# Kernel tuning notes

Hardware: AMD Instinct MI355X
Metric: run time of the kernel (lower is better)

Reference implementation:

```python
import jax, jax.numpy as jnp
import numpy as np
from jax import lax

B, CIN, COUT, LAT, H, W, K = 16, 512, 512, 512, 32, 32, 3


def setup_inputs() -> dict:
    key = jax.random.key(0)
    k1, k2, k3, k4 = jax.random.split(key, 4)
    return {
        "x": jax.random.normal(k1, (B, CIN, H, W), jnp.float32),
        "w": jax.random.normal(k2, (B, LAT), jnp.float32),
        "weight": jax.random.normal(k3, (COUT, CIN, K, K), jnp.float32) * 0.05,
        "bias": jnp.zeros((1, COUT, 1, 1), jnp.float32),
        "affine_w": jax.random.normal(k4, (CIN, LAT), jnp.float32) * 0.02,
        "affine_b": jnp.zeros((CIN,), jnp.float32),
    }


def _blur_kernel():
    # make_kernel([1,3,3,1]) * upsample_factor**2 (factor=2)
    k = jnp.array([1.0, 3.0, 3.0, 1.0], jnp.float32)
    k = k[None, :] * k[:, None]
    k = k / k.sum()
    return k * 4.0  # (4, 4)


def reference(x, w, weight, bias, affine_w, affine_b):
    bs = x.shape[0]
    # style: affine(w) + 1  -> (B, Cin)
    s = w @ affine_w.T + affine_b + 1.0
    # per-sample modulated weights (B, Cout, Cin, K, K)
    wm = s[:, None, :, None, None] * weight[None]
    # demodulation
    d = lax.rsqrt(jnp.sum(wm * wm, axis=(2, 3, 4)) + 1e-8)  # (B, Cout)
    wm = d[:, :, None, None, None] * wm
    # fused grouped conv_transpose2d(stride=2, padding=0) expressed as a
    # direct cross-correlation with lhs_dilation=2, pad K-1, spatially
    # flipped per-sample kernels, feature_group_count = batch.
    rhs = jnp.flip(wm, (-2, -1)).reshape(bs * COUT, CIN, K, K)
    xr = x.reshape(1, bs * CIN, H, W)
    y = lax.conv_general_dilated(
        xr, rhs, window_strides=(1, 1),
        padding=((K - 1, K - 1), (K - 1, K - 1)),
        lhs_dilation=(2, 2),
        dimension_numbers=("NCHW", "OIHW", "NCHW"),
        feature_group_count=bs)
    Ho, Wo = y.shape[2], y.shape[3]  # 65, 65
    y = y.reshape(bs, COUT, Ho, Wo)
    # upfirdn2d blur: up=1, down=1, pad=(1,1); torch correlates with the
    # flipped kernel, i.e. a true convolution -> depthwise correlate flipped k.
    bk = jnp.flip(_blur_kernel(), (0, 1))
    dw = jnp.broadcast_to(bk[None, None], (COUT, 1, 4, 4))
    y = lax.conv_general_dilated(
        y, dw, window_strides=(1, 1), padding=((1, 1), (1, 1)),
        dimension_numbers=("NCHW", "OIHW", "NCHW"),
        feature_group_count=COUT)  # -> (B, Cout, 64, 64)
    return y + bias
```

## Files before the change

kernel.cpp:

```cpp
#include <hip/hip_runtime.h>

#define CIN  512
#define COUT 512
#define LAT  512
#define NB   16

typedef __attribute__((ext_vector_type(8))) short bf16x8;
typedef __attribute__((ext_vector_type(4))) float f32x4;

__device__ __forceinline__ unsigned short f2bf(float f) {
    unsigned int u = __builtin_bit_cast(unsigned int, f);
    u += 0x7FFFu + ((u >> 16) & 1u);
    return (unsigned short)(u >> 16);
}

__global__ void k_style(const float* __restrict__ w, const float* __restrict__ aw,
                        const float* __restrict__ ab, float* __restrict__ s) {
    int b = blockIdx.x, ci = threadIdx.x;
    __shared__ float wl[LAT];
    wl[ci] = w[b * LAT + ci];
    __syncthreads();
    const float4* awr = (const float4*)(aw + (size_t)ci * LAT);
    float acc = 0.f;
#pragma unroll 4
    for (int l = 0; l < LAT / 4; ++l) {
        float4 a4 = awr[l];
        const float* wp = &wl[l * 4];
        acc += a4.x * wp[0] + a4.y * wp[1] + a4.z * wp[2] + a4.w * wp[3];
    }
    s[b * CIN + ci] = acc + ab[ci] + 1.0f;
}

__global__ void k_wsq(const float* __restrict__ weight, float* __restrict__ wsq) {
    int co = blockIdx.x, ci = threadIdx.x;
    const float* p = weight + ((size_t)co * CIN + ci) * 9;
    float a = 0.f;
#pragma unroll
    for (int k = 0; k < 9; ++k) a += p[k] * p[k];
    wsq[co * CIN + ci] = a;
}

__global__ void k_demod(const float* __restrict__ s, const float* __restrict__ wsq,
                        float* __restrict__ d) {
    int b = blockIdx.x, co = threadIdx.x;
    __shared__ float s2[CIN];
    float sv = s[b * CIN + co];
    s2[co] = sv * sv;
    __syncthreads();
    const float4* wr = (const float4*)(wsq + (size_t)co * CIN);
    float acc = 0.f;
#pragma unroll 4
    for (int i = 0; i < CIN / 4; ++i) {
        float4 v = wr[i];
        const float* sp = &s2[i * 4];
        acc += v.x * sp[0] + v.y * sp[1] + v.z * sp[2] + v.w * sp[3];
    }
    d[b * COUT + co] = rsqrtf(acc + 1e-8f);
}

__global__ void k_prepw(const float* __restrict__ weight, unsigned short* __restrict__ A9) {
    int co = blockIdx.x, t = threadIdx.x;
    __shared__ float wl[CIN * 9];
    const float* wp = weight + (size_t)co * CIN * 9;
    for (int i = t; i < CIN * 9; i += 256) wl[i] = wp[i];
    __syncthreads();
    unsigned short* ap = A9 + (size_t)co * 9 * CIN;
    for (int i = t; i < CIN * 9; i += 256) {
        int kk = i >> 9, ci = i & 511;
        ap[i] = f2bf(wl[ci * 9 + kk]);
    }
}

__global__ void k_prepx(const float* __restrict__ x, const float* __restrict__ s,
                        unsigned short* __restrict__ XT) {
    int blk = blockIdx.x;
    int b = blk >> 7, pt = (blk >> 3) & 15, ct = blk & 7;
    int p0 = pt * 64, ci0 = ct * 64;
    __shared__ float xt[64][65];
    __shared__ float ss[64];
    int t = threadIdx.x;
    if (t < 64) ss[t] = s[b * CIN + ci0 + t];
    const float* xb = x + ((size_t)(b * CIN + ci0)) * 1024 + p0;
#pragma unroll
    for (int rr = 0; rr < 4; ++rr) {
        int i = rr * 16 + (t >> 4), j = (t & 15) * 4;
        float4 v = *(const float4*)(xb + (size_t)i * 1024 + j);
        xt[i][j] = v.x; xt[i][j + 1] = v.y; xt[i][j + 2] = v.z; xt[i][j + 3] = v.w;
    }
    __syncthreads();
    unsigned short* xo = XT + ((size_t)(b * 1024 + p0)) * CIN + ci0;
#pragma unroll
    for (int rr = 0; rr < 4; ++rr) {
        int jj = rr * 16 + (t >> 4);
        int c4 = (t & 15) * 4;
        ushort4 o;
        o.x = f2bf(xt[c4][jj] * ss[c4]);
        o.y = f2bf(xt[c4 + 1][jj] * ss[c4 + 1]);
        o.z = f2bf(xt[c4 + 2][jj] * ss[c4 + 2]);
        o.w = f2bf(xt[c4 + 3][jj] * ss[c4 + 3]);
        *(ushort4*)(xo + (size_t)jj * CIN + c4) = o;
    }
}

__device__ __forceinline__ void gload16(const void* g, void* l) {
    __builtin_amdgcn_global_load_lds(
        (const __attribute__((address_space(1))) void*)g,
        (__attribute__((address_space(3))) void*)l, 16, 0, 0);
}

__device__ __forceinline__ unsigned int swz_goff(unsigned int o) {
    unsigned int row = o >> 6, kb = o & 63u;
    unsigned int kbx = kb ^ (((row >> 1) & 3u) << 4);
    return row * 1024u + kbx;
}

__launch_bounds__(256, 3)
__global__ void k_gemm(const unsigned short* __restrict__ A9,
                       const unsigned short* __restrict__ XT,
                       _Float16* __restrict__ C, int Ns) {
    __shared__ unsigned short smem[8192];
    const int t = threadIdx.x;
    const int bm = blockIdx.x, bn = blockIdx.y;

    const unsigned int o0 = (unsigned)t * 16u;
    const unsigned int o1 = o0 + 4096u;
    char* lA0 = (char*)smem + ((t >> 6) * 1024);
    char* lA1 = lA0 + 4096;
    char* lB0 = lA0 + 8192;
    char* lB1 = lA1 + 8192;
    const char* gA = (const char*)A9 + (size_t)bm * 128 * 1024;
    const char* gB = (const char*)XT + (size_t)bn * 128 * 1024;
    const char* pA0 = gA + swz_goff(o0);
    const char* pA1 = gA + swz_goff(o1);
    const char* pB0 = gB + swz_goff(o0);
    const char* pB1 = gB + swz_goff(o1);

    const int lane = t & 63, w = t >> 6, wr = w >> 1, wc = w & 1;
    const int lrow = lane & 15;
    const unsigned int kbx = (unsigned)(((lane >> 4) << 4) ^ (((lrow >> 1) & 3) << 4));
    unsigned int offA[4], offB[4];
#pragma unroll
    for (int f = 0; f < 4; ++f) {
        offA[f] = (unsigned)((wr * 64 + f * 16 + lrow) * 64) + kbx;
        offB[f] = 8192u + (unsigned)((wc * 64 + f * 16 + lrow) * 64) + kbx;
    }

    f32x4 acc[4][4];
#pragma unroll
    for (int i = 0; i < 4; ++i)
#pragma unroll
        for (int j = 0; j < 4; ++j) acc[i][j] = (f32x4){0.f, 0.f, 0.f, 0.f};

    for (int it = 0; it < 16; ++it) {
        __syncthreads();
        gload16(pA0, lA0); gload16(pA1, lA1);
        gload16(pB0, lB0); gload16(pB1, lB1);
        pA0 += 64; pA1 += 64; pB0 += 64; pB1 += 64;
        __syncthreads();
        bf16x8 a[4], b[4];
#pragma unroll
        for (int f = 0; f < 4; ++f) a[f] = *(const bf16x8*)((const char*)smem + offA[f]);
#pragma unroll
        for (int f = 0; f < 4; ++f) b[f] = *(const bf16x8*)((const char*)smem + offB[f]);
#pragma unroll
        for (int mf = 0; mf < 4; ++mf)
#pragma unroll
            for (int nf = 0; nf < 4; ++nf)
                acc[mf][nf] = __builtin_amdgcn_mfma_f32_16x16x32_bf16(
                    a[mf], b[nf], acc[mf][nf], 0, 0, 0);
    }

    const int mg0 = bm * 128 + wr * 64 + (lane >> 4) * 4;
    const int ng0 = bn * 128 + wc * 64 + (lane & 15);
#pragma unroll
    for (int mf = 0; mf < 4; ++mf)
#pragma unroll
        for (int j = 0; j < 4; ++j) {
            size_t row = (size_t)(mg0 + mf * 16 + j) * (size_t)Ns;
#pragma unroll
            for (int nf = 0; nf < 4; ++nf)
                C[row + ng0 + nf * 16] = (_Float16)acc[mf][nf][j];
        }
}

__global__ void k_scat(const _Float16* __restrict__ C, const float* __restrict__ dmod,
                       const float* __restrict__ bias, float* __restrict__ out,
                       int b0, int Ns) {
    const int blk = blockIdx.x;
    const int bl = blk >> 9, co = blk & 511, b = b0 + bl;
    const int t = threadIdx.x;
    __shared__ _Float16 ct[9][1024];
    __shared__ float ys[67 * 68];

    const _Float16* Cb = C + (size_t)(co * 9) * (size_t)Ns + bl * 1024;
#pragma unroll
    for (int k = 0; k < 9; ++k)
        ((ushort4*)ct[k])[t] = ((const ushort4*)(Cb + (size_t)k * Ns))[t];
    for (int i = t; i < 67 * 68; i += 256) ys[i] = 0.f;
    __syncthreads();

    for (int id = t; id < 65 * 65; id += 256) {
        int oy = id / 65, ox = id - oy * 65;
        int kys[2], iys[2], nk = 0;
        if (oy & 1) { kys[0] = 1; iys[0] = oy >> 1; nk = 1; }
        else {
            int h = oy >> 1;
            if (h < 32) { kys[0] = 0; iys[0] = h; nk = 1; }
            if (h >= 1) { kys[nk] = 2; iys[nk] = h - 1; nk++; }
        }
        int kxs[2], ixs[2], nx = 0;
        if (ox & 1) { kxs[0] = 1; ixs[0] = ox >> 1; nx = 1; }
        else {
            int h = ox >> 1;
            if (h < 32) { kxs[0] = 0; ixs[0] = h; nx = 1; }
            if (h >= 1) { kxs[nx] = 2; ixs[nx] = h - 1; nx++; }
        }
        float v = 0.f;
        for (int ia = 0; ia < nk; ++ia)
            for (int ic = 0; ic < nx; ++ic)
                v += (float)ct[kys[ia] * 3 + kxs[ic]][iys[ia] * 32 + ixs[ic]];
        ys[(oy + 1) * 68 + ox + 1] = v;
    }
    __syncthreads();

    const float dv = dmod[b * COUT + co];
    const float bv = bias[co];
    const int px = t & 63, py0 = t >> 6;
    float* orow = out + ((size_t)b * COUT + co) * 4096;
    const float kv[4] = {0.25f, 0.75f, 0.75f, 0.25f};
#pragma unroll 4
    for (int j = 0; j < 16; ++j) {
        int py = py0 + 4 * j;
        float sum = 0.f;
#pragma unroll
        for (int u = 0; u < 4; ++u) {
            const float* yr = &ys[(py + u) * 68 + px];
            float rs = yr[0] * kv[0] + yr[1] * kv[1] + yr[2] * kv[2] + yr[3] * kv[3];
            sum = fmaf(rs, kv[u], sum);
        }
        orow[py * 64 + px] = dv * sum + bv;
    }
}

extern "C" void kernel_launch(void* const* d_in, const int* in_sizes, int n_in,
                              void* d_out, int out_size, void* d_ws, size_t ws_size,
                              hipStream_t stream) {
    const float* x      = (const float*)d_in[0];
    const float* w      = (const float*)d_in[1];
    const float* weight = (const float*)d_in[2];
    const float* bias   = (const float*)d_in[3];
    const float* aw     = (const float*)d_in[4];
    const float* ab     = (const float*)d_in[5];
    float* out = (float*)d_out;

    char* wsb = (char*)d_ws;
    float* s            = (float*)wsb;
    float* dmod         = (float*)(wsb + 32768);
    float* wsq          = (float*)(wsb + 65536);
    unsigned short* A9  = (unsigned short*)(wsb + 1114112);
    unsigned short* XT  = (unsigned short*)(wsb + 5832704);
    _Float16* C         = (_Float16*)(wsb + 22609920);
    const size_t cbase  = 22609920;

    size_t avail = ws_size > cbase ? ws_size - cbase : 0;
    int nbc = 16;
    while (nbc > 1 && (size_t)4608 * 1024 * (size_t)nbc * 2 > avail) nbc >>= 1;

    k_style<<<NB, 512, 0, stream>>>(w, aw, ab, s);
    k_wsq<<<COUT, 512, 0, stream>>>(weight, wsq);
    k_demod<<<NB, 512, 0, stream>>>(s, wsq, dmod);
    k_prepw<<<COUT, 256, 0, stream>>>(weight, A9);
    k_prepx<<<2048, 256, 0, stream>>>(x, s, XT);

    const int Ns = nbc * 1024;
    for (int bb = 0; bb < NB; bb += nbc) {
        k_gemm<<<dim3(36, nbc * 8), 256, 0, stream>>>(A9, XT + (size_t)bb * 1024 * CIN, C, Ns);
        k_scat<<<nbc * 512, 256, 0, stream>>>(C, dmod, bias, out, bb, Ns);
    }
}
```

Baseline: 451.7 us.

## Double-buffer GEMM LDS loads, widen tiles, and separabilize the post-processing blur

The GEMM now runs 512 threads on a 128x256 tile and double-buffers the async global-to-LDS loads, which removes one barrier per K step and overlaps loading with MFMA work. The scatter/blur kernel is replaced by a version that folds the stride-2 transposed-conv scatter into a horizontal blur pass, stores fp16 intermediates in LDS, and then runs a vertical pass that writes float2 outputs. The batch chunk drops from 16 to 8, so the GEMM/post pair launches twice. The cost is more LDS per block and extra fp16 rounding of the intermediates, and the launch bounds may raise register pressure.

New measurement: 720.8 us. 59.6% more time.

```diff
diff --git a/kernel.cpp b/kernel.cpp
--- a/kernel.cpp
+++ b/kernel.cpp
@@ -108,37 +108,28 @@
         (__attribute__((address_space(3))) void*)l, 16, 0, 0);
 }
 
-__device__ __forceinline__ unsigned int swz_goff(unsigned int o) {
-    unsigned int row = o >> 6, kb = o & 63u;
-    unsigned int kbx = kb ^ (((row >> 1) & 3u) << 4);
-    return row * 1024u + kbx;
-}
-
-__launch_bounds__(256, 3)
+__launch_bounds__(512, 6)
 __global__ void k_gemm(const unsigned short* __restrict__ A9,
                        const unsigned short* __restrict__ XT,
                        _Float16* __restrict__ C, int Ns) {
-    __shared__ unsigned short smem[8192];
+    __shared__ unsigned short smem[24576];
     const int t = threadIdx.x;
     const int bm = blockIdx.x, bn = blockIdx.y;
-
-    const unsigned int o0 = (unsigned)t * 16u;
-    const unsigned int o1 = o0 + 4096u;
-    char* lA0 = (char*)smem + ((t >> 6) * 1024);
-    char* lA1 = lA0 + 4096;
-    char* lB0 = lA0 + 8192;
-    char* lB1 = lA1 + 8192;
-    const char* gA = (const char*)A9 + (size_t)bm * 128 * 1024;
-    const char* gB = (const char*)XT + (size_t)bn * 128 * 1024;
-    const char* pA0 = gA + swz_goff(o0);
-    const char* pA1 = gA + swz_goff(o1);
-    const char* pB0 = gB + swz_goff(o0);
-    const char* pB1 = gB + swz_goff(o1);
-
-    const int lane = t & 63, w = t >> 6, wr = w >> 1, wc = w & 1;
+    const int w = t >> 6, lane = t & 63;
+    const int wr = w >> 2, wc = w & 3;
     const int lrow = lane & 15;
-    const unsigned int kbx = (unsigned)(((lane >> 4) << 4) ^ (((lrow >> 1) & 3) << 4));
-    unsigned int offA[4], offB[4];
+
+    const int rowT = t >> 2;
+    const unsigned kbT = ((unsigned)(t & 3) << 4) ^ ((((unsigned)rowT >> 1) & 3u) << 4);
+    const char* pA  = (const char*)A9 + (size_t)(bm * 128 + rowT) * 1024 + kbT;
+    const char* pB1 = (const char*)XT + (size_t)(bn * 256 + rowT) * 1024 + kbT;
+    const char* pB2 = pB1 + (size_t)128 * 1024;
+    char* dA  = (char*)smem + (w << 10);
+    char* dB1 = dA + 8192;
+    char* dB2 = dA + 16384;
+
+    const unsigned kbx = ((unsigned)(lane >> 4) << 4) ^ ((((unsigned)lrow >> 1) & 3u) << 4);
+    unsigned offA[4], offB[4];
 #pragma unroll
     for (int f = 0; f < 4; ++f) {
         offA[f] = (unsigned)((wr * 64 + f * 16 + lrow) * 64) + kbx;
@@ -151,27 +142,34 @@
 #pragma unroll
         for (int j = 0; j < 4; ++j) acc[i][j] = (f32x4){0.f, 0.f, 0.f, 0.f};
 
+    gload16(pA, dA); gload16(pB1, dB1); gload16(pB2, dB2);
+    pA += 64; pB1 += 64; pB2 += 64;
+
+    int selOff = 0;
     for (int it = 0; it < 16; ++it) {
         __syncthreads();
-        gload16(pA0, lA0); gload16(pA1, lA1);
-        gload16(pB0, lB0); gload16(pB1, lB1);
-        pA0 += 64; pA1 += 64; pB0 += 64; pB1 += 64;
-        __syncthreads();
+        if (it < 15) {
+            int nOff = selOff ^ 24576;
+            gload16(pA, dA + nOff); gload16(pB1, dB1 + nOff); gload16(pB2, dB2 + nOff);
+            pA += 64; pB1 += 64; pB2 += 64;
+        }
+        const char* rb = (const char*)smem + selOff;
         bf16x8 a[4], b[4];
 #pragma unroll
-        for (int f = 0; f < 4; ++f) a[f] = *(const bf16x8*)((const char*)smem + offA[f]);
-#pragma unroll
-        for (int f = 0; f < 4; ++f) b[f] = *(const bf16x8*)((const char*)smem + offB[f]);
+        for (int f = 0; f < 4; ++f) a[f] = *(const bf16x8*)(rb + offA[f]);
+#pragma unroll
+        for (int f = 0; f < 4; ++f) b[f] = *(const bf16x8*)(rb + offB[f]);
 #pragma unroll
         for (int mf = 0; mf < 4; ++mf)
 #pragma unroll
             for (int nf = 0; nf < 4; ++nf)
                 acc[mf][nf] = __builtin_amdgcn_mfma_f32_16x16x32_bf16(
                     a[mf], b[nf], acc[mf][nf], 0, 0, 0);
+        selOff ^= 24576;
     }
 
     const int mg0 = bm * 128 + wr * 64 + (lane >> 4) * 4;
-    const int ng0 = bn * 128 + wc * 64 + (lane & 15);
+    const int ng0 = bn * 256 + wc * 64 + lrow;
 #pragma unroll
     for (int mf = 0; mf < 4; ++mf)
 #pragma unroll
@@ -183,62 +181,95 @@
         }
 }
 
-__global__ void k_scat(const _Float16* __restrict__ C, const float* __restrict__ dmod,
+__device__ __forceinline__ float2 up2(unsigned u) {
+    _Float16 lo = __builtin_bit_cast(_Float16, (unsigned short)(u & 0xffffu));
+    _Float16 hi = __builtin_bit_cast(_Float16, (unsigned short)(u >> 16));
+    return make_float2((float)lo, (float)hi);
+}
+
+__launch_bounds__(512, 6)
+__global__ void k_post(const _Float16* __restrict__ C, const float* __restrict__ dmod,
                        const float* __restrict__ bias, float* __restrict__ out,
                        int b0, int Ns) {
     const int blk = blockIdx.x;
     const int bl = blk >> 9, co = blk & 511, b = b0 + bl;
     const int t = threadIdx.x;
-    __shared__ _Float16 ct[9][1024];
-    __shared__ float ys[67 * 68];
-
-    const _Float16* Cb = C + (size_t)(co * 9) * (size_t)Ns + bl * 1024;
-#pragma unroll
-    for (int k = 0; k < 9; ++k)
-        ((ushort4*)ct[k])[t] = ((const ushort4*)(Cb + (size_t)k * Ns))[t];
-    for (int i = t; i < 67 * 68; i += 256) ys[i] = 0.f;
-    __syncthreads();
-
-    for (int id = t; id < 65 * 65; id += 256) {
-        int oy = id / 65, ox = id - oy * 65;
-        int kys[2], iys[2], nk = 0;
-        if (oy & 1) { kys[0] = 1; iys[0] = oy >> 1; nk = 1; }
-        else {
-            int h = oy >> 1;
-            if (h < 32) { kys[0] = 0; iys[0] = h; nk = 1; }
-            if (h >= 1) { kys[nk] = 2; iys[nk] = h - 1; nk++; }
-        }
-        int kxs[2], ixs[2], nx = 0;
-        if (ox & 1) { kxs[0] = 1; ixs[0] = ox >> 1; nx = 1; }
-        else {
-            int h = ox >> 1;
-            if (h < 32) { kxs[0] = 0; ixs[0] = h; nx = 1; }
-            if (h >= 1) { kxs[nx] = 2; ixs[nx] = h - 1; nx++; }
-        }
-        float v = 0.f;
-        for (int ia = 0; ia < nk; ++ia)
-            for (int ic = 0; ic < nx; ++ic)
-                v += (float)ct[kys[ia] * 3 + kxs[ic]][iys[ia] * 32 + ixs[ic]];
-        ys[(oy + 1) * 68 + ox + 1] = v;
+    __shared__ __align__(16) char pool[31904];
+    _Float16* taps = (_Float16*)pool;
+
+    const char* Cb = (const char*)(C + (size_t)(co * 9) * (size_t)Ns + bl * 1024);
+    const size_t nsb = (size_t)Ns * 2;
+    int4 v0 = *(const int4*)(Cb + (size_t)(t >> 7) * nsb + (t & 127) * 16);
+    int4 v1 = *(const int4*)(Cb + (size_t)((t + 512) >> 7) * nsb + ((t + 512) & 127) * 16);
+    int4 v2;
+    if (t < 128) v2 = *(const int4*)(Cb + (size_t)((t + 1024) >> 7) * nsb + ((t + 1024) & 127) * 16);
+    if (t < 198) {
+        int ky = t / 66, rem = t % 66;
+        int rowoff = (rem < 33) ? 0 : 4356;
+        int ci = (rem < 33) ? rem : rem - 33;
+        ((unsigned*)(pool + 18432 + ky * 4488 + rowoff))[ci] = 0u;
+    }
+    *(int4*)(pool + t * 16) = v0;
+    *(int4*)(pool + 8192 + t * 16) = v1;
+    if (t < 128) *(int4*)(pool + 16384 + t * 16) = v2;
+    __syncthreads();
+
+#pragma unroll
+    for (int i = 0; i < 3; ++i) {
+        int tau = t + 512 * i;
+        int ky = tau >> 9, rem = tau & 511;
+        int iy = rem >> 4, q = rem & 15, c = 2 * q;
+        const _Float16* T0 = taps + (ky * 3) * 1024 + iy * 32;
+        const _Float16* T1 = T0 + 1024;
+        const _Float16* T2 = T0 + 2048;
+        int cm = (q > 0) ? c - 1 : 0;
+        int cp = (q < 15) ? c + 2 : 31;
+        float t0a = (float)T0[c], t0b = (float)T0[c + 1];
+        float t1a = (float)T1[c], t1b = (float)T1[c + 1];
+        float t2a = (float)T2[c], t2b = (float)T2[c + 1];
+        float t1m = (q > 0) ? (float)T1[cm] : 0.f;
+        float t2m = (q > 0) ? (float)T2[cm] : 0.f;
+        float t0c = (q < 15) ? (float)T0[cp] : 0.f;
+        float t1c = (q < 15) ? (float)T1[cp] : 0.f;
+        float E0 = t0a + t2m, E1 = t0b + t2a, E2 = t0c + t2b;
+        float h0 = 0.25f * t1m + 0.75f * E0 + 0.75f * t1a + 0.25f * E1;
+        float h1 = 0.25f * E0 + 0.75f * t1a + 0.75f * E1 + 0.25f * t1b;
+        float h2 = 0.25f * t1a + 0.75f * E1 + 0.75f * t1b + 0.25f * E2;
+        float h3 = 0.25f * E1 + 0.75f * t1b + 0.75f * E2 + 0.25f * t1c;
+        unsigned* Hrow = (unsigned*)(pool + 18432 + ky * 4488 + (iy + 1) * 132);
+        unsigned p01 = (unsigned)__builtin_bit_cast(unsigned short, (_Float16)h0) |
+                       ((unsigned)__builtin_bit_cast(unsigned short, (_Float16)h1) << 16);
+        unsigned p23 = (unsigned)__builtin_bit_cast(unsigned short, (_Float16)h2) |
+                       ((unsigned)__builtin_bit_cast(unsigned short, (_Float16)h3) << 16);
+        Hrow[2 * q] = p01;
+        Hrow[2 * q + 1] = p23;
     }
     __syncthreads();
 
     const float dv = dmod[b * COUT + co];
     const float bv = bias[co];
-    const int px = t & 63, py0 = t >> 6;
-    float* orow = out + ((size_t)b * COUT + co) * 4096;
-    const float kv[4] = {0.25f, 0.75f, 0.75f, 0.25f};
-#pragma unroll 4
-    for (int j = 0; j < 16; ++j) {
-        int py = py0 + 4 * j;
-        float sum = 0.f;
-#pragma unroll
-        for (int u = 0; u < 4; ++u) {
-            const float* yr = &ys[(py + u) * 68 + px];
-            float rs = yr[0] * kv[0] + yr[1] * kv[1] + yr[2] * kv[2] + yr[3] * kv[3];
-            sum = fmaf(rs, kv[u], sum);
-        }
-        orow[py * 64 + px] = dv * sum + bv;
+    float* oplane = out + ((size_t)b * COUT + co) * 4096;
+#pragma unroll
+    for (int i = 0; i < 4; ++i) {
+        int tau = t + 512 * i;
+        int py = tau >> 5, pr = tau & 31, px0 = 2 * pr;
+        int m = py >> 1, par = py & 1;
+        const char* Hb = pool + 18432 + px0 * 2;
+        float2 h0a = up2(*(const unsigned*)(Hb + (m + 1) * 132));
+        float2 h0b = up2(*(const unsigned*)(Hb + (m + 2) * 132));
+        int r1 = m + par;
+        float2 h1a = up2(*(const unsigned*)(Hb + 4488 + r1 * 132));
+        float2 h1b = up2(*(const unsigned*)(Hb + 4488 + (r1 + 1) * 132));
+        float2 h2a = up2(*(const unsigned*)(Hb + 8976 + m * 132));
+        float2 h2b = up2(*(const unsigned*)(Hb + 8976 + (m + 1) * 132));
+        float wP = par ? 0.25f : 0.75f;
+        float wQ = par ? 0.75f : 0.25f;
+        float s0 = wP * h0a.x + wQ * h0b.x + wQ * h1a.x + wP * h1b.x + wP * h2a.x + wQ * h2b.x;
+        float s1 = wP * h0a.y + wQ * h0b.y + wQ * h1a.y + wP * h1b.y + wP * h2a.y + wQ * h2b.y;
+        float2 o;
+        o.x = fmaf(dv, s0, bv);
+        o.y = fmaf(dv, s1, bv);
+        *(float2*)(oplane + py * 64 + px0) = o;
     }
 }
 
@@ -263,7 +294,7 @@
     const size_t cbase  = 22609920;
 
     size_t avail = ws_size > cbase ? ws_size - cbase : 0;
-    int nbc = 16;
+    int nbc = 8;
     while (nbc > 1 && (size_t)4608 * 1024 * (size_t)nbc * 2 > avail) nbc >>= 1;
 
     k_style<<<NB, 512, 0, stream>>>(w, aw, ab, s);
@@ -274,7 +305,7 @@
 
     const int Ns = nbc * 1024;
     for (int bb = 0; bb < NB; bb += nbc) {
-        k_gemm<<<dim3(36, nbc * 8), 256, 0, stream>>>(A9, XT + (size_t)bb * 1024 * CIN, C, Ns);
-        k_scat<<<nbc * 512, 256, 0, stream>>>(C, dmod, bias, out, bb, Ns);
-    }
-}
+        k_gemm<<<dim3(36, nbc * 4), 512, 0, stream>>>(A9, XT + (size_t)bb * 1024 * CIN, C, Ns);
+        k_post<<<nbc * 512, 512, 0, stream>>>(C, dmod, bias, out, bb, Ns);
+    }
+}
```
